# Kernel tuning notes

Hardware: AMD Instinct MI355X
Metric: run time of the kernel (lower is better)

The kernel has to match this reference:

```python
import jax, jax.numpy as jnp
import numpy as np

# dims: B=1 graph, N nodes, H heads, D head dim, M random features, K gumbel samples
N, E, H, D, M, K, IN = 50000, 800000, 4, 64, 30, 10, 128
TAU = 0.25
EPS = 1e-6


def _kernel_feat(data, proj, is_query):
    # FAVOR+ positive softmax kernel features. data [B,N,H,D], proj [M,D] -> [B,N,H,M]
    d = data.shape[-1]
    data = data * (float(d) ** -0.25)
    ratio = float(proj.shape[0]) ** -0.5
    dash = jnp.einsum('bnhd,md->bnhm', data, proj)
    diag = jnp.sum(data * data, axis=-1, keepdims=True) * 0.5
    if is_query:
        stab = jnp.max(dash, axis=-1, keepdims=True)
    else:
        stab = jnp.max(jnp.max(dash, axis=-1, keepdims=True), axis=-3, keepdims=True)
    return ratio * (jnp.exp(dash - diag - stab) + EPS)


def setup_inputs():
    key = jax.random.key(0)
    ks = jax.random.split(key, 10)
    def lin(k, o, i):
        return jax.random.normal(k, (o, i), jnp.float32) / np.sqrt(i)
    return {
        'z': jax.random.normal(ks[0], (1, N, IN), jnp.float32),
        'edge_index': jax.random.randint(ks[1], (2, E), 0, N),
        'Wq_w': lin(ks[2], H * D, IN), 'Wq_b': jnp.zeros((H * D,), jnp.float32),
        'Wk_w': lin(ks[3], H * D, IN), 'Wk_b': jnp.zeros((H * D,), jnp.float32),
        'Wv_w': lin(ks[4], H * D, IN), 'Wv_b': jnp.zeros((H * D,), jnp.float32),
        'Wo_w': lin(ks[5], D, H * D), 'Wo_b': jnp.zeros((D,), jnp.float32),
        'b_rb': jnp.full((1, H), 0.1, jnp.float32),  # rb_order=1 relational-bias scalars
        'proj': jax.random.normal(ks[6], (M, D), jnp.float32),  # random-feature projection
        # pre-sampled Gumbel noise, already divided by tau and clamped at 20 as in torch
        'gumbels': jnp.minimum(jax.random.gumbel(ks[7], (N, 1, H, K), jnp.float32) / TAU, 20.0),
    }


def reference(z, edge_index, Wq_w, Wq_b, Wk_w, Wk_b, Wv_w, Wv_b, Wo_w, Wo_b, b_rb, proj, gumbels):
    B, Nn = z.shape[0], z.shape[1]
    inv_sqrt_tau = 1.0 / np.sqrt(TAU)
    q = (jnp.einsum('bni,oi->bno', z, Wq_w) + Wq_b).reshape(B, Nn, H, D)
    k = (jnp.einsum('bni,oi->bno', z, Wk_w) + Wk_b).reshape(B, Nn, H, D)
    v = (jnp.einsum('bni,oi->bno', z, Wv_w) + Wv_b).reshape(B, Nn, H, D)
    qp = jnp.transpose(_kernel_feat(q * inv_sqrt_tau, proj, True), (1, 0, 2, 3))   # [N,B,H,M]
    kp = jnp.transpose(_kernel_feat(k * inv_sqrt_tau, proj, False), (1, 0, 2, 3))  # [N,B,H,M]
    vp = jnp.transpose(v, (1, 0, 2, 3))                                             # [N,B,H,D]
    # Gumbel-perturbed keys: [N,B,H,K,M]
    ktg = kp[:, :, :, None, :] * jnp.exp(gumbels)[..., None]
    kvs = jnp.einsum('nbhkm,nbhd->bhkmd', ktg, vp)
    z_num = jnp.einsum('nbhm,bhkmd->nbhkd', qp, kvs)        # [N,B,H,K,D]
    z_den = jnp.einsum('nbhm,bhkm->nbhk', qp, jnp.sum(ktg, axis=0))
    z_next = jnp.transpose(jnp.mean(z_num / z_den[..., None], axis=3), (1, 0, 2, 3))  # [B,N,H,D]
    # edge attention weights A_weight [B,E,H]
    start, end = edge_index[0], edge_index[1]
    e_num = jnp.einsum('ebhm,ebhm->ebh', qp[end], kp[start])
    norm = jnp.einsum('nbhm,bhm->nbh', qp, jnp.sum(kp, axis=0))
    A_weight = jnp.transpose(e_num, (1, 0, 2)) / jnp.transpose(norm[end], (1, 0, 2))
    # relational bias (rb_order=1): sym-normalized sparse conv with per-head sigmoid scalar
    row, col = start, end
    d_in = jnp.zeros((Nn,), jnp.float32).at[col].add(1.0)
    d_out = jnp.zeros((Nn,), jnp.float32).at[row].add(1.0)
    coeff = jax.nn.sigmoid(b_rb[0])[None, :] * (jax.lax.rsqrt(d_in[col]) * jax.lax.rsqrt(d_out[row]))[:, None]  # [E,H]
    msg = v[0, row] * coeff[:, :, None]                      # [E,H,D]
    conv = jax.ops.segment_sum(msg, col, num_segments=Nn)[None]  # [1,N,H,D]
    z_next = z_next + conv
    out = jnp.einsum('bnf,of->bno', z_next.reshape(B, Nn, H * D), Wo_w) + Wo_b  # [B,N,D]
    return out, A_weight
```

## Files before the change

kernel.cpp:

```cpp
#include <hip/hip_runtime.h>

#define NN 50000
#define EE 800000
#define IND 128
#define NCOL 1024
#define KM 320
#define M30 30
#define RATIO 0.1825741858f
#define EPSF 1e-6f
#define QKSCALE 0.7071067812f
#define VTS 50176
#define KVSNB 196
#define AST 136

typedef __attribute__((ext_vector_type(8))) short bf16x8;
typedef __attribute__((ext_vector_type(4))) float f32x4;

__device__ __forceinline__ unsigned f2s(float f) {
    unsigned u = __float_as_uint(f);
    return (u & 0x80000000u) ? ~u : (u | 0x80000000u);
}
__device__ __forceinline__ float s2f(unsigned s) {
    return __uint_as_float((s & 0x80000000u) ? (s & 0x7fffffffu) : ~s);
}
__device__ __forceinline__ unsigned short f2bf(float f) {
    unsigned u = __float_as_uint(f);
    unsigned r = u + 0x7fffu + ((u >> 16) & 1u);
    return (unsigned short)(r >> 16);
}
__device__ __forceinline__ float bf2f(unsigned short h) {
    return __uint_as_float(((unsigned)h) << 16);
}

__global__ void k_prep(const float* __restrict__ Wq, const float* __restrict__ Wqb,
                       const float* __restrict__ Wk, const float* __restrict__ Wkb,
                       const float* __restrict__ Wv, const float* __restrict__ Wvb,
                       const float* __restrict__ Wo, const float* __restrict__ proj,
                       float* __restrict__ Wt, float* __restrict__ bext, float* __restrict__ WoT) {
    int i = blockIdx.x;
    int t = threadIdx.x;
    Wt[i*NCOL + t]       = QKSCALE * Wq[t*IND + i];
    Wt[i*NCOL + 256 + t] = QKSCALE * Wk[t*IND + i];
    Wt[i*NCOL + 512 + t] = Wv[t*IND + i];
    {
        const float* W = (t < 128) ? Wq : Wk;
        int c = (t < 128) ? t : (t - 128);
        int h = c >> 5, m = c & 31;
        float val = 0.f;
        if (m < M30) {
            for (int d = 0; d < 64; ++d)
                val += QKSCALE * W[(h*64+d)*IND + i] * proj[m*64 + d];
        }
        Wt[i*NCOL + 768 + t] = val;
    }
    if (t < 128) {
        int f = i*2 + (t >> 6);
        int o = t & 63;
        WoT[f*64 + o] = Wo[o*256 + f];
    }
    if (i == 0) {
        bext[t]       = QKSCALE * Wqb[t];
        bext[256 + t] = QKSCALE * Wkb[t];
        bext[512 + t] = Wvb[t];
        const float* Bb = (t < 128) ? Wqb : Wkb;
        int c = (t < 128) ? t : (t - 128);
        int h = c >> 5, m = c & 31;
        float val = 0.f;
        if (m < M30) {
            for (int d = 0; d < 64; ++d)
                val += QKSCALE * Bb[h*64+d] * proj[m*64 + d];
        }
        bext[768 + t] = val;
    }
}

__global__ void k_prep2(const float* __restrict__ Wt, unsigned short* __restrict__ Wcb) {
    int idx = blockIdx.x*256 + threadIdx.x;
    int col = idx >> 7, k = idx & 127;
    float f = Wt[k*NCOL + col];
    unsigned short hi = f2bf(f);
    unsigned short lo = f2bf(f - bf2f(hi));
    Wcb[col*128 + k] = hi;
    Wcb[131072 + col*128 + k] = lo;
}

__global__ void k_ztail(unsigned* __restrict__ vT32) {
    int idx = blockIdx.x*256 + threadIdx.x;
    int row = idx / 88, c = idx - row*88;
    vT32[(size_t)row * (VTS/2) + (50000/2) + c] = 0u;
}

__global__ __launch_bounds__(256) void k_qkv_mfma(const float* __restrict__ z,
                      const unsigned short* __restrict__ Wcb, const float* __restrict__ bext,
                      float* __restrict__ vbuf, float* __restrict__ qp, float* __restrict__ kpb,
                      unsigned* __restrict__ stab) {
    __shared__ __align__(16) unsigned short a_hi[128*AST];
    __shared__ float diag_l[2][4][128];
    int t = threadIdx.x;
    int n0 = blockIdx.x * 128;
    int w = t >> 6, lane = t & 63;
    #pragma unroll
    for (int half = 0; half < 2; ++half) {
        int node = (t >> 2) + half*64;
        int ks = (t & 3) * 32;
        bool ok = (n0 + node) < NN;
        const float* zr = z + (size_t)(n0 + node)*IND + ks;
        unsigned hbuf[16];
        #pragma unroll
        for (int c = 0; c < 8; ++c) {
            float4 v = ok ? *(const float4*)(zr + c*4) : make_float4(0.f,0.f,0.f,0.f);
            hbuf[c*2]   = (unsigned)f2bf(v.x) | ((unsigned)f2bf(v.y) << 16);
            hbuf[c*2+1] = (unsigned)f2bf(v.z) | ((unsigned)f2bf(v.w) << 16);
        }
        uint4* hp = (uint4*)(&a_hi[node*AST + ks]);
        #pragma unroll
        for (int c = 0; c < 4; ++c)
            hp[c] = make_uint4(hbuf[c*4], hbuf[c*4+1], hbuf[c*4+2], hbuf[c*4+3]);
    }
    __syncthreads();
    int arow = lane & 15;
    int ao = (lane >> 4) * 8;
    for (int c = 0; c < 4; ++c) {
        int colbase = c*256 + w*64;
        f32x4 acc[8][4];
        #pragma unroll
        for (int mt = 0; mt < 8; ++mt)
            #pragma unroll
            for (int nt = 0; nt < 4; ++nt)
                acc[mt][nt] = (f32x4){0.f,0.f,0.f,0.f};
        #pragma unroll
        for (int ks = 0; ks < 4; ++ks) {
            int ko = ks*32 + ao;
            bf16x8 Ah[8];
            #pragma unroll
            for (int mt = 0; mt < 8; ++mt)
                Ah[mt] = *(const bf16x8*)(&a_hi[(mt*16 + arow)*AST + ko]);
            #pragma unroll
            for (int nt = 0; nt < 4; ++nt) {
                const unsigned short* bp = Wcb + (size_t)(colbase + nt*16 + arow)*128 + ko;
                bf16x8 Bh = *(const bf16x8*)bp;
                bf16x8 Bl = *(const bf16x8*)(bp + 131072);
                #pragma unroll
                for (int mt = 0; mt < 8; ++mt) {
                    acc[mt][nt] = __builtin_amdgcn_mfma_f32_16x16x32_bf16(Ah[mt], Bh, acc[mt][nt], 0, 0, 0);
                    acc[mt][nt] = __builtin_amdgcn_mfma_f32_16x16x32_bf16(Ah[mt], Bl, acc[mt][nt], 0, 0, 0);
                }
            }
        }
        float bv[4];
        #pragma unroll
        for (int nt = 0; nt < 4; ++nt) bv[nt] = bext[colbase + nt*16 + arow];
        #pragma unroll
        for (int mt = 0; mt < 8; ++mt)
            #pragma unroll
            for (int nt = 0; nt < 4; ++nt)
                #pragma unroll
                for (int r = 0; r < 4; ++r)
                    acc[mt][nt][r] += bv[nt];
        if (c < 2) {
            #pragma unroll
            for (int mt = 0; mt < 8; ++mt) {
                #pragma unroll
                for (int r = 0; r < 4; ++r) {
                    float s = 0.f;
                    #pragma unroll
                    for (int nt = 0; nt < 4; ++nt) s += acc[mt][nt][r]*acc[mt][nt][r];
                    s += __shfl_xor(s, 1); s += __shfl_xor(s, 2);
                    s += __shfl_xor(s, 4); s += __shfl_xor(s, 8);
                    if (arow == 0) diag_l[c][w][mt*16 + (lane>>4)*4 + r] = 0.5f*s;
                }
            }
        } else if (c == 2) {
            #pragma unroll
            for (int mt = 0; mt < 8; ++mt)
                #pragma unroll
                for (int r = 0; r < 4; ++r) {
                    int node = n0 + mt*16 + (lane>>4)*4 + r;
                    if (node < NN) {
                        #pragma unroll
                        for (int nt = 0; nt < 4; ++nt)
                            vbuf[(size_t)node*256 + w*64 + nt*16 + arow] = acc[mt][nt][r];
                    }
                }
        } else {
            int hh = (w & 1) * 2;
            if (w < 2) {
                #pragma unroll
                for (int p = 0; p < 2; ++p) {
                    int h = hh + p;
                    #pragma unroll
                    for (int mt = 0; mt < 8; ++mt) {
                        #pragma unroll
                        for (int r = 0; r < 4; ++r) {
                            int row = mt*16 + (lane>>4)*4 + r;
                            float dg = diag_l[0][h][row];
                            float mx = fmaxf(acc[mt][2*p][r],
                                             (arow < 14) ? acc[mt][2*p+1][r] : -3.0e38f);
                            mx = fmaxf(mx, __shfl_xor(mx, 1)); mx = fmaxf(mx, __shfl_xor(mx, 2));
                            mx = fmaxf(mx, __shfl_xor(mx, 4)); mx = fmaxf(mx, __shfl_xor(mx, 8));
                            int node = n0 + row;
                            if (node < NN) {
                                #pragma unroll
                                for (int q2 = 0; q2 < 2; ++q2) {
                                    int m = q2*16 + arow;
                                    float val = 0.f;
                                    if (m < M30)
                                        val = RATIO * (__expf(acc[mt][2*p+q2][r] - dg - mx) + EPSF);
                                    qp[(size_t)node*128 + h*32 + m] = val;
                                }
                            }
                        }
                    }
                }
            } else {
                #pragma unroll
                for (int p = 0; p < 2; ++p) {
                    int h = hh + p;
                    float smax = -3.0e38f;
                    #pragma unroll
                    for (int mt = 0; mt < 8; ++mt) {
                        #pragma unroll
                        for (int r = 0; r < 4; ++r) {
                            int row = mt*16 + (lane>>4)*4 + r;
                            float dg = diag_l[1][h][row];
                            int node = n0 + row;
                            if (node < NN) {
                                #pragma unroll
                                for (int q2 = 0; q2 < 2; ++q2) {
                                    int m = q2*16 + arow;
                                    float d = acc[mt][2*p+q2][r];
                                    bool valid = (m < M30);
                                    kpb[(size_t)node*128 + h*32 + m] = valid ? (d - dg) : 0.f;
                                    if (valid) smax = fmaxf(smax, d);
                                }
                            }
                        }
                    }
                    smax = fmaxf(smax, __shfl_xor(smax, 1));  smax = fmaxf(smax, __shfl_xor(smax, 2));
                    smax = fmaxf(smax, __shfl_xor(smax, 4));  smax = fmaxf(smax, __shfl_xor(smax, 8));
                    smax = fmaxf(smax, __shfl_xor(smax, 16)); smax = fmaxf(smax, __shfl_xor(smax, 32));
                    if (lane == 0) atomicMax(&stab[h], f2s(smax));
                }
            }
        }
        __syncthreads();
    }
}

__global__ __launch_bounds__(256) void k_vt(const float* __restrict__ vbuf,
                      unsigned short* __restrict__ vT) {
    __shared__ unsigned short tile[64][72];
    int t = threadIdx.x;
    int n0 = blockIdx.x * 64;
    int c0 = blockIdx.y * 64;
    {
        int node = t >> 2, cs = (t & 3) * 16;
        bool ok = (n0 + node) < NN;
        const float* vr = vbuf + (size_t)(n0 + node)*256 + c0 + cs;
        #pragma unroll
        for (int cc = 0; cc < 4; ++cc) {
            float4 v = ok ? *(const float4*)(vr + cc*4) : make_float4(0.f,0.f,0.f,0.f);
            unsigned u0 = (unsigned)f2bf(v.x) | ((unsigned)f2bf(v.y) << 16);
            unsigned u1 = (unsigned)f2bf(v.z) | ((unsigned)f2bf(v.w) << 16);
            *(unsigned*)(&tile[node][cs + cc*4])     = u0;
            *(unsigned*)(&tile[node][cs + cc*4 + 2]) = u1;
        }
    }
    __syncthreads();
    {
        int d = t >> 2, ns = (t & 3) * 16;
        unsigned ob[8];
        #pragma unroll
        for (int i = 0; i < 8; ++i) {
            unsigned short a = tile[ns + i*2][d];
            unsigned short b = tile[ns + i*2 + 1][d];
            ob[i] = (unsigned)a | ((unsigned)b << 16);
        }
        unsigned short* op = vT + (size_t)(c0 + d)*VTS + n0 + ns;
        *(uint4*)(op)     = make_uint4(ob[0], ob[1], ob[2], ob[3]);
        *(uint4*)(op + 8) = make_uint4(ob[4], ob[5], ob[6], ob[7]);
    }
}

__global__ void k_deg(const int* __restrict__ ei, int* __restrict__ din, int* __restrict__ dout) {
    int e = blockIdx.x*256 + threadIdx.x;
    if (e < EE) {
        atomicAdd(&dout[ei[e]], 1);
        atomicAdd(&din[ei[EE + e]], 1);
    }
}

__global__ void k_scan_part(const int* __restrict__ din, int* __restrict__ bsum) {
    __shared__ int red[256];
    int t = threadIdx.x;
    int i = blockIdx.x*256 + t;
    red[t] = (i < NN) ? din[i] : 0;
    __syncthreads();
    for (int off = 128; off >= 1; off >>= 1) {
        if (t < off) red[t] += red[t+off];
        __syncthreads();
    }
    if (t == 0) bsum[blockIdx.x] = red[0];
}
__global__ void k_scan_top(const int* __restrict__ bsum, int* __restrict__ boff) {
    if (threadIdx.x == 0) {
        int acc = 0;
        for (int b = 0; b < 196; ++b) { boff[b] = acc; acc += bsum[b]; }
    }
}
__global__ void k_scan_fin(const int* __restrict__ din, const int* __restrict__ boff,
                           int* __restrict__ offsets, int* __restrict__ cursor,
                           const int* __restrict__ dout_, float* __restrict__ rsd) {
    __shared__ int s[256];
    int t = threadIdx.x;
    int i = blockIdx.x*256 + t;
    if (i < NN) {
        int d = dout_[i];
        rsd[i] = d > 0 ? rsqrtf((float)d) : 0.f;
    }
    int v = (i < NN) ? din[i] : 0;
    s[t] = v;
    __syncthreads();
    for (int off = 1; off < 256; off <<= 1) {
        int add = (t >= off) ? s[t-off] : 0;
        __syncthreads();
        s[t] += add;
        __syncthreads();
    }
    int excl = s[t] - v + boff[blockIdx.x];
    if (i < NN) { offsets[i] = excl; cursor[i] = excl; }
    if (i == NN-1) offsets[NN] = excl + v;
}

__global__ void k_scatter(const int* __restrict__ ei, int* __restrict__ cursor,
                          int2* __restrict__ csr_pack) {
    int e = blockIdx.x*256 + threadIdx.x;
    if (e < EE) {
        int col = ei[EE + e];
        int pos = atomicAdd(&cursor[col], 1);
        csr_pack[pos] = make_int2(ei[e], e);
    }
}

__global__ void k_kp(const float* __restrict__ kpb, const unsigned* __restrict__ stab,
                     float* __restrict__ kp_sum, unsigned short* __restrict__ kp_bf) {
    __shared__ float red[256];
    int t = threadIdx.x;
    int hm = t & 127;
    int h = hm >> 5, m = hm & 31;
    float st = s2f(stab[h]);
    float ksum = 0.f;
    const int total = NN*128;
    for (int idx = blockIdx.x*256 + t; idx < total; idx += gridDim.x*256) {
        float val = kpb[idx];
        float kpv = 0.f;
        if (m < M30) kpv = RATIO * (__expf(val - st) + EPSF);
        kp_bf[idx] = f2bf(kpv);
        ksum += kpv;
    }
    red[t] = ksum;
    __syncthreads();
    if (t < 128) atomicAdd(&kp_sum[hm], red[t] + red[t+128]);
}

__global__ __launch_bounds__(256) void k_kvs(const unsigned short* __restrict__ kp_bf,
                      const float* __restrict__ g, const unsigned short* __restrict__ vT,
                      float* __restrict__ kvs, float* __restrict__ ktg) {
    __shared__ __align__(16) unsigned short w_l[320*40];
    __shared__ __align__(16) unsigned short v_l[64*40];
    __shared__ __align__(16) float eg_l[10][36];
    __shared__ float kp_lf[32][33];
    int t = threadIdx.x;
    int h = blockIdx.y;
    int n0b = blockIdx.x * 256;
    int lane = t & 63;
    int wb = (t >> 6) * 80;
    int arow = lane & 15;
    int acol = (lane >> 4) * 8;
    f32x4 acc[5][4];
    #pragma unroll
    for (int kt = 0; kt < 5; ++kt)
        #pragma unroll
        for (int dt = 0; dt < 4; ++dt)
            acc[kt][dt] = (f32x4){0.f, 0.f, 0.f, 0.f};
    float wsum0 = 0.f, wsum1 = 0.f;
    int k0 = t >> 5, m0 = t & 31;
    int k1 = 8 + (t >> 5), m1 = t & 31;

    for (int st = 0; st < 8; ++st) {
        int n0 = n0b + st * 32;
        __syncthreads();
        #pragma unroll
        for (int i = 0; i < 2; ++i) {
            int flat = t + i*256;
            if (flat < 320) {
                int kk = flat % 10, n = flat / 10;
                float e = 0.f;
                if (n0 + n < NN) e = __expf(g[(size_t)(n0+n)*40 + h*10 + kk]);
                eg_l[kk][n] = e;
            }
        }
        {
            int d = t >> 2, seg = t & 3;
            uint4 vv = *(const uint4*)(vT + (size_t)(h*64 + d)*VTS + n0 + seg*8);
            *(uint4*)(&v_l[d*40 + seg*8]) = vv;
        }
        if (t < 128) {
            int n = t >> 2, seg = t & 3;
            int gn = n0 + n;
            if (gn < NN) {
                uint4 kv = *(const uint4*)(kp_bf + (size_t)gn*128 + h*32 + seg*8);
                unsigned uu[4] = {kv.x, kv.y, kv.z, kv.w};
                #pragma unroll
                for (int j = 0; j < 4; ++j) {
                    kp_lf[n][seg*8 + j*2]     = __uint_as_float(uu[j] << 16);
                    kp_lf[n][seg*8 + j*2 + 1] = __uint_as_float(uu[j] & 0xFFFF0000u);
                }
            } else {
                #pragma unroll
                for (int j = 0; j < 8; ++j) kp_lf[n][seg*8 + j] = 0.f;
            }
        }
        __syncthreads();
        {
            {
                unsigned dw[16];
                float s = 0.f;
                #pragma unroll
                for (int c = 0; c < 16; ++c) {
                    float kpa = kp_lf[c*2][m0];
                    float kpc = kp_lf[c*2+1][m0];
                    unsigned ua = __float_as_uint(kpa * eg_l[k0][c*2]);
                    unsigned ub = __float_as_uint(kpc * eg_l[k0][c*2+1]);
                    s += __uint_as_float(ua & 0xFFFF0000u) + __uint_as_float(ub & 0xFFFF0000u);
                    dw[c] = (ua >> 16) | (ub & 0xFFFF0000u);
                }
                wsum0 += s;
                uint4* wp = (uint4*)(&w_l[t*40]);
                wp[0] = make_uint4(dw[0], dw[1], dw[2],  dw[3]);
                wp[1] = make_uint4(dw[4], dw[5], dw[6],  dw[7]);
                wp[2] = make_uint4(dw[8], dw[9], dw[10], dw[11]);
                wp[3] = make_uint4(dw[12],dw[13],dw[14], dw[15]);
            }
            if (t < 64) {
                unsigned dw[16];
                float s = 0.f;
                #pragma unroll
                for (int c = 0; c < 16; ++c) {
                    float kpa = kp_lf[c*2][m1];
                    float kpc = kp_lf[c*2+1][m1];
                    unsigned ua = __float_as_uint(kpa * eg_l[k1][c*2]);
                    unsigned ub = __float_as_uint(kpc * eg_l[k1][c*2+1]);
                    s += __uint_as_float(ua & 0xFFFF0000u) + __uint_as_float(ub & 0xFFFF0000u);
                    dw[c] = (ua >> 16) | (ub & 0xFFFF0000u);
                }
                wsum1 += s;
                uint4* wp = (uint4*)(&w_l[(t + 256)*40]);
                wp[0] = make_uint4(dw[0], dw[1], dw[2],  dw[3]);
                wp[1] = make_uint4(dw[4], dw[5], dw[6],  dw[7]);
                wp[2] = make_uint4(dw[8], dw[9], dw[10], dw[11]);
                wp[3] = make_uint4(dw[12],dw[13],dw[14], dw[15]);
            }
        }
        __syncthreads();
        bf16x8 Bf[4];
        #pragma unroll
        for (int dt = 0; dt < 4; ++dt)
            Bf[dt] = *(const bf16x8*)(&v_l[(dt*16 + arow)*40 + acol]);
        #pragma unroll
        for (int kt = 0; kt < 5; ++kt) {
            bf16x8 Af = *(const bf16x8*)(&w_l[(wb + kt*16 + arow)*40 + acol]);
            #pragma unroll
            for (int dt = 0; dt < 4; ++dt)
                acc[kt][dt] = __builtin_amdgcn_mfma_f32_16x16x32_bf16(Af, Bf[dt], acc[kt][dt], 0, 0, 0);
        }
    }
    {
        int orow = (lane >> 4) * 4;
        int ocol = lane & 15;
        float* kb = kvs + h*KM*64;
        #pragma unroll
        for (int kt = 0; kt < 5; ++kt)
            #pragma unroll
            for (int dt = 0; dt < 4; ++dt)
                #pragma unroll
                for (int r = 0; r < 4; ++r)
                    atomicAdd(&kb[(wb + kt*16 + orow + r)*64 + dt*16 + ocol], acc[kt][dt][r]);
        atomicAdd(&ktg[h*KM + t], wsum0);
        if (t < 64) atomicAdd(&ktg[h*KM + 256 + t], wsum1);
    }
}

__global__ __launch_bounds__(256) void k_znext(const float* __restrict__ qp, const float* __restrict__ kvs,
                        const float* __restrict__ ktg, const float* __restrict__ kp_sum,
                        float* __restrict__ znext, unsigned short* __restrict__ qpn_bf) {
    int t = threadIdx.x;
    int n = blockIdx.x*256 + t;
    int h = blockIdx.y;
    if (n >= NN) return;
    float q[32];
    const float* qb = qp + (size_t)n*128 + h*32;
    #pragma unroll
    for (int c = 0; c < 8; ++c) {
        float4 v4 = *(const float4*)(qb + c*4);
        q[c*4+0]=v4.x; q[c*4+1]=v4.y; q[c*4+2]=v4.z; q[c*4+3]=v4.w;
    }
    const float* ks = kp_sum + h*32;
    float norm = 0.f;
    #pragma unroll
    for (int m = 0; m < 32; ++m) norm = fmaf(q[m], ks[m], norm);
    float rn = 1.f / norm;
    #pragma unroll
    for (int m = 0; m < 32; ++m) q[m] *= rn;
    {
        unsigned ob[16];
        #pragma unroll
        for (int c = 0; c < 16; ++c)
            ob[c] = (unsigned)f2bf(q[c*2]) | ((unsigned)f2bf(q[c*2+1]) << 16);
        unsigned short* qo = qpn_bf + (size_t)n*128 + h*32;
        *(uint4*)(qo)      = make_uint4(ob[0],  ob[1],  ob[2],  ob[3]);
        *(uint4*)(qo + 8)  = make_uint4(ob[4],  ob[5],  ob[6],  ob[7]);
        *(uint4*)(qo + 16) = make_uint4(ob[8],  ob[9],  ob[10], ob[11]);
        *(uint4*)(qo + 24) = make_uint4(ob[12], ob[13], ob[14], ob[15]);
    }
    const float* kvh = kvs + h*KM*64;
    const float* kth = ktg + h*KM;
    float* zo = znext + (size_t)n*256 + h*64;
    for (int dc = 0; dc < 4; ++dc) {
        float ms[16];
        #pragma unroll
        for (int d = 0; d < 16; ++d) ms[d] = 0.f;
        for (int k = 0; k < 10; ++k) {
            float den = 0.f;
            #pragma unroll
            for (int m = 0; m < 32; ++m) den = fmaf(q[m], kth[k*32+m], den);
            float rd = 1.f / (den * 10.f);
            const float* base = kvh + k*2048 + dc*16;
            #pragma unroll
            for (int m = 0; m < 32; ++m) {
                float qm = q[m] * rd;
                #pragma unroll
                for (int d = 0; d < 16; ++d)
                    ms[d] = fmaf(qm, base[m*64 + d], ms[d]);
            }
        }
        #pragma unroll
        for (int d = 0; d < 16; ++d) zo[dc*16 + d] = ms[d];
    }
}

__global__ __launch_bounds__(256) void k_convedge(const int* __restrict__ offsets,
                        const int2* __restrict__ csr_pack,
                        const int* __restrict__ din, const unsigned short* __restrict__ vr,
                        const unsigned short* __restrict__ kp_bf,
                        const unsigned short* __restrict__ qpn_bf,
                        const float* __restrict__ brb, float* __restrict__ znext,
                        float* __restrict__ A) {
    __shared__ unsigned short qpn_l[4][128];
    int t = threadIdx.x;
    int w = t >> 6, lane = t & 63;
    int col = blockIdx.x*4 + w;
    if (lane < 8) {
        uint4 q4 = *(const uint4*)(qpn_bf + (size_t)col*128 + lane*8);
        *(uint4*)(&qpn_l[w][lane*8]) = q4;
    }
    __syncthreads();
    int s0 = offsets[col], s1 = offsets[col+1];
    int hq = (lane & 31) >> 3;
    float qv0, qv1, qv2, qv3;
    {
        ushort4 qq = *(const ushort4*)(&qpn_l[w][hq*32 + (lane & 7)*4]);
        qv0 = bf2f(qq.x); qv1 = bf2f(qq.y); qv2 = bf2f(qq.z); qv3 = bf2f(qq.w);
    }
    bool dowrite = (lane < 32) && ((lane & 7) == 0);
    float a0 = 0.f, a1 = 0.f, a2 = 0.f, a3 = 0.f;
    int j = s0;
    for (; j + 2 <= s1; j += 2) {
        int2 p0 = csr_pack[j];
        int2 p1 = csr_pack[j+1];
        ushort4 u0 = *(const ushort4*)(vr + (size_t)p0.x*256 + lane*4);
        ushort4 u1 = *(const ushort4*)(vr + (size_t)p1.x*256 + lane*4);
        ushort4 k0 = *(const ushort4*)(kp_bf + (size_t)p0.x*128 + (lane & 31)*4);
        ushort4 k1 = *(const ushort4*)(kp_bf + (size_t)p1.x*128 + (lane & 31)*4);
        a0 += bf2f(u0.x) + bf2f(u1.x);
        a1 += bf2f(u0.y) + bf2f(u1.y);
        a2 += bf2f(u0.z) + bf2f(u1.z);
        a3 += bf2f(u0.w) + bf2f(u1.w);
        float d0 = qv0*bf2f(k0.x) + qv1*bf2f(k0.y) + qv2*bf2f(k0.z) + qv3*bf2f(k0.w);
        float d1 = qv0*bf2f(k1.x) + qv1*bf2f(k1.y) + qv2*bf2f(k1.z) + qv3*bf2f(k1.w);
        d0 += __shfl_xor(d0, 1); d1 += __shfl_xor(d1, 1);
        d0 += __shfl_xor(d0, 2); d1 += __shfl_xor(d1, 2);
        d0 += __shfl_xor(d0, 4); d1 += __shfl_xor(d1, 4);
        if (dowrite) {
            A[(size_t)p0.y*4 + hq] = d0;
            A[(size_t)p1.y*4 + hq] = d1;
        }
    }
    if (j < s1) {
        int2 p0 = csr_pack[j];
        ushort4 u0 = *(const ushort4*)(vr + (size_t)p0.x*256 + lane*4);
        ushort4 k0 = *(const ushort4*)(kp_bf + (size_t)p0.x*128 + (lane & 31)*4);
        a0 += bf2f(u0.x); a1 += bf2f(u0.y); a2 += bf2f(u0.z); a3 += bf2f(u0.w);
        float d0 = qv0*bf2f(k0.x) + qv1*bf2f(k0.y) + qv2*bf2f(k0.z) + qv3*bf2f(k0.w);
        d0 += __shfl_xor(d0, 1); d0 += __shfl_xor(d0, 2); d0 += __shfl_xor(d0, 4);
        if (dowrite) A[(size_t)p0.y*4 + hq] = d0;
    }
    if (s0 == s1) return;
    int h = lane >> 4;
    float sig = 1.f / (1.f + __expf(-brb[h]));
    float sc = sig * rsqrtf((float)din[col]);
    float* zp = znext + (size_t)col*256 + lane*4;
    float4 zv = *(float4*)zp;
    zv.x += sc*a0; zv.y += sc*a1; zv.z += sc*a2; zv.w += sc*a3;
    *(float4*)zp = zv;
}

__global__ __launch_bounds__(256) void k_vr(const float* __restrict__ vbuf,
                      const float* __restrict__ rsd, unsigned short* __restrict__ vr) {
    int t = threadIdx.x;
    int row = blockIdx.x*4 + (t >> 6);
    int lane = t & 63;
    float rs = rsd[row];
    float4 v4 = *(const float4*)(vbuf + (size_t)row*256 + lane*4);
    ushort4 o;
    o.x = f2bf(rs * v4.x);
    o.y = f2bf(rs * v4.y);
    o.z = f2bf(rs * v4.z);
    o.w = f2bf(rs * v4.w);
    *(ushort4*)(vr + (size_t)row*256 + lane*4) = o;
}

__global__ __launch_bounds__(256) void k_out(const float* __restrict__ znext, const float* __restrict__ WoT,
                      const float* __restrict__ Wob, float* __restrict__ out) {
    int n = blockIdx.x*256 + threadIdx.x;
    if (n >= NN) return;
    float acc[64];
    #pragma unroll
    for (int o = 0; o < 64; ++o) acc[o] = Wob[o];
    const float* zr = znext + (size_t)n*256;
    for (int fc = 0; fc < 64; ++fc) {
        float4 z4 = *(const float4*)(zr + fc*4);
        float zz[4] = {z4.x, z4.y, z4.z, z4.w};
        #pragma unroll
        for (int j = 0; j < 4; ++j) {
            const float* wr = WoT + (fc*4+j)*64;
            #pragma unroll
            for (int o = 0; o < 64; ++o)
                acc[o] = fmaf(zz[j], wr[o], acc[o]);
        }
    }
    float* ob = out + (size_t)n*64;
    #pragma unroll
    for (int o = 0; o < 64; ++o) ob[o] = acc[o];
}

extern "C" void kernel_launch(void* const* d_in, const int* in_sizes, int n_in,
                              void* d_out, int out_size, void* d_ws, size_t ws_size,
                              hipStream_t stream) {
    const float* z    = (const float*)d_in[0];
    const int*   ei   = (const int*)d_in[1];
    const float* Wq   = (const float*)d_in[2];
    const float* Wqb  = (const float*)d_in[3];
    const float* Wk   = (const float*)d_in[4];
    const float* Wkb  = (const float*)d_in[5];
    const float* Wv   = (const float*)d_in[6];
    const float* Wvb  = (const float*)d_in[7];
    const float* Wo   = (const float*)d_in[8];
    const float* Wob  = (const float*)d_in[9];
    const float* brb  = (const float*)d_in[10];
    const float* proj = (const float*)d_in[11];
    const float* g    = (const float*)d_in[12];
    float* out = (float*)d_out;
    float* A   = out + (size_t)NN*64;
    float* ws  = (float*)d_ws;

    float* Wt      = ws;
    float* bext    = ws + 131072;
    float* WoT     = ws + 132096;
    float* kvs     = ws + 148480;
    float* ktg     = ws + 230400;
    float* kp_sum  = ws + 231680;
    unsigned* stab = (unsigned*)(ws + 231808);
    int* din       = (int*)(ws + 231812);
    int* dout_     = (int*)(ws + 281812);
    float* vbuf    = ws + 331840;
    float* qp      = ws + 13131840;
    float* kpb     = ws + 19531840;
    float* znext   = ws + 25931840;
    int* offsets   = (int*)(ws + 38731840);
    int* cursor    = (int*)(ws + 38781844);
    int* bsum      = (int*)(ws + 38831844);
    int* boff      = (int*)(ws + 38832040);
    float* rsd     = ws + 38832236;
    unsigned short* Wcb = (unsigned short*)(ws + 38882240);
    unsigned short* vT     = (unsigned short*)znext;
    int2* csr_pack         = (int2*)kpb;
    float* A_scratch       = kpb + 1600000;
    unsigned short* vr     = (unsigned short*)qp;
    unsigned short* kp_bf  = (unsigned short*)A;
    unsigned short* qpn_bf = (unsigned short*)out;

    hipMemsetAsync(ws + 148480, 0, (size_t)(331840 - 148480)*sizeof(float), stream);
    k_prep<<<128, 256, 0, stream>>>(Wq, Wqb, Wk, Wkb, Wv, Wvb, Wo, proj, Wt, bext, WoT);
    k_prep2<<<512, 256, 0, stream>>>(Wt, Wcb);
    k_ztail<<<88, 256, 0, stream>>>((unsigned*)vT);
    k_qkv_mfma<<<391, 256, 0, stream>>>(z, Wcb, bext, vbuf, qp, kpb, stab);
    k_deg<<<3125, 256, 0, stream>>>(ei, din, dout_);
    k_scan_part<<<196, 256, 0, stream>>>(din, bsum);
    k_scan_top<<<1, 64, 0, stream>>>(bsum, boff);
    k_scan_fin<<<196, 256, 0, stream>>>(din, boff, offsets, cursor, dout_, rsd);
    k_kp<<<512, 256, 0, stream>>>(kpb, stab, kp_sum, kp_bf);
    k_scatter<<<3125, 256, 0, stream>>>(ei, cursor, csr_pack);
    k_vt<<<dim3(782, 4), 256, 0, stream>>>(vbuf, vT);
    k_kvs<<<dim3(KVSNB, 4), 256, 0, stream>>>(kp_bf, g, vT, kvs, ktg);
    k_znext<<<dim3(196,4), 256, 0, stream>>>(qp, kvs, ktg, kp_sum, znext, qpn_bf);
    k_vr<<<12500, 256, 0, stream>>>(vbuf, rsd, vr);
    k_convedge<<<12500, 256, 0, stream>>>(offsets, csr_pack, din, vr, kp_bf,
                                          qpn_bf, brb, znext, A_scratch);
    k_out<<<196, 256, 0, stream>>>(znext, WoT, Wob, out);
    hipMemcpyAsync(A, A_scratch, (size_t)EE*4*sizeof(float), hipMemcpyDeviceToDevice, stream);
}
```

Measured before the change: 756.2 us.

## Compute z_next numerator with bf16 MFMA over scaled query features

Replaces the scalar per-node k_znext loop with an MFMA kernel. Each block builds a 64-node tile of per-sample scaled query features (q/den) in bf16 shared memory and multiplies it against a transposed bf16 copy of kvs produced by a new small conversion kernel. The mean over the K samples folds into the 320-long reduction. This targets a large FMA-bound loop with heavy redundant loads of kvs, at the cost of bf16 rounding of kvs and of the scaled queries, plus one extra launch.

```diff
diff --git a/kernel.cpp b/kernel.cpp
--- a/kernel.cpp
+++ b/kernel.cpp
@@ -491,61 +491,98 @@
     }
 }
 
-__global__ __launch_bounds__(256) void k_znext(const float* __restrict__ qp, const float* __restrict__ kvs,
+__global__ void k_kvsbf(const float* __restrict__ kvs, unsigned short* __restrict__ kvs_bfT) {
+    int idx = blockIdx.x*256 + threadIdx.x;
+    int h = idx / 20480;
+    int rem = idx - h*20480;
+    int d = rem / 320;
+    int km = rem - d*320;
+    kvs_bfT[idx] = f2bf(kvs[(size_t)h*20480 + km*64 + d]);
+}
+
+__global__ __launch_bounds__(256) void k_znext_mfma(const float* __restrict__ qp,
+                        const unsigned short* __restrict__ kvs_bfT,
                         const float* __restrict__ ktg, const float* __restrict__ kp_sum,
                         float* __restrict__ znext, unsigned short* __restrict__ qpn_bf) {
-    int t = threadIdx.x;
-    int n = blockIdx.x*256 + t;
+    __shared__ __align__(16) unsigned short A_l[64*328];
+    __shared__ float ktg_l[320];
+    __shared__ float ksum_l[32];
+    int t = threadIdx.x;
     int h = blockIdx.y;
-    if (n >= NN) return;
-    float q[32];
-    const float* qb = qp + (size_t)n*128 + h*32;
-    #pragma unroll
-    for (int c = 0; c < 8; ++c) {
-        float4 v4 = *(const float4*)(qb + c*4);
-        q[c*4+0]=v4.x; q[c*4+1]=v4.y; q[c*4+2]=v4.z; q[c*4+3]=v4.w;
-    }
-    const float* ks = kp_sum + h*32;
-    float norm = 0.f;
-    #pragma unroll
-    for (int m = 0; m < 32; ++m) norm = fmaf(q[m], ks[m], norm);
-    float rn = 1.f / norm;
-    #pragma unroll
-    for (int m = 0; m < 32; ++m) q[m] *= rn;
+    int n0 = blockIdx.x * 64;
+    ktg_l[t] = ktg[h*KM + t];
+    if (t < 64) ktg_l[256 + t] = ktg[h*KM + 256 + t];
+    if (t < 32) ksum_l[t] = kp_sum[h*32 + t];
+    __syncthreads();
     {
-        unsigned ob[16];
-        #pragma unroll
-        for (int c = 0; c < 16; ++c)
-            ob[c] = (unsigned)f2bf(q[c*2]) | ((unsigned)f2bf(q[c*2+1]) << 16);
-        unsigned short* qo = qpn_bf + (size_t)n*128 + h*32;
-        *(uint4*)(qo)      = make_uint4(ob[0],  ob[1],  ob[2],  ob[3]);
-        *(uint4*)(qo + 8)  = make_uint4(ob[4],  ob[5],  ob[6],  ob[7]);
-        *(uint4*)(qo + 16) = make_uint4(ob[8],  ob[9],  ob[10], ob[11]);
-        *(uint4*)(qo + 24) = make_uint4(ob[12], ob[13], ob[14], ob[15]);
-    }
-    const float* kvh = kvs + h*KM*64;
-    const float* kth = ktg + h*KM;
-    float* zo = znext + (size_t)n*256 + h*64;
-    for (int dc = 0; dc < 4; ++dc) {
-        float ms[16];
-        #pragma unroll
-        for (int d = 0; d < 16; ++d) ms[d] = 0.f;
+        int node = t >> 2, p = t & 3;
+        int n = n0 + node;
+        bool ok = (n < NN);
+        float q8[8];
+        if (ok) {
+            const float* qb = qp + (size_t)n*128 + h*32 + p*8;
+            float4 a = *(const float4*)(qb);
+            float4 b = *(const float4*)(qb + 4);
+            q8[0]=a.x; q8[1]=a.y; q8[2]=a.z; q8[3]=a.w;
+            q8[4]=b.x; q8[5]=b.y; q8[6]=b.z; q8[7]=b.w;
+        } else {
+            #pragma unroll
+            for (int j = 0; j < 8; ++j) q8[j] = 0.f;
+        }
+        float part = 0.f;
+        #pragma unroll
+        for (int j = 0; j < 8; ++j) part = fmaf(q8[j], ksum_l[p*8 + j], part);
+        part += __shfl_xor(part, 1); part += __shfl_xor(part, 2);
+        float rn = ok ? (1.f / part) : 0.f;
+        #pragma unroll
+        for (int j = 0; j < 8; ++j) q8[j] *= rn;
+        if (ok) {
+            unsigned ob[4];
+            #pragma unroll
+            for (int c = 0; c < 4; ++c)
+                ob[c] = (unsigned)f2bf(q8[c*2]) | ((unsigned)f2bf(q8[c*2+1]) << 16);
+            *(uint4*)(qpn_bf + (size_t)n*128 + h*32 + p*8) = make_uint4(ob[0], ob[1], ob[2], ob[3]);
+        }
+        #pragma unroll
         for (int k = 0; k < 10; ++k) {
-            float den = 0.f;
-            #pragma unroll
-            for (int m = 0; m < 32; ++m) den = fmaf(q[m], kth[k*32+m], den);
-            float rd = 1.f / (den * 10.f);
-            const float* base = kvh + k*2048 + dc*16;
-            #pragma unroll
-            for (int m = 0; m < 32; ++m) {
-                float qm = q[m] * rd;
-                #pragma unroll
-                for (int d = 0; d < 16; ++d)
-                    ms[d] = fmaf(qm, base[m*64 + d], ms[d]);
-            }
-        }
-        #pragma unroll
-        for (int d = 0; d < 16; ++d) zo[dc*16 + d] = ms[d];
+            float dp = 0.f;
+            #pragma unroll
+            for (int j = 0; j < 8; ++j) dp = fmaf(q8[j], ktg_l[k*32 + p*8 + j], dp);
+            dp += __shfl_xor(dp, 1); dp += __shfl_xor(dp, 2);
+            float rd = ok ? (1.f / (dp * 10.f)) : 0.f;
+            unsigned ob[4];
+            #pragma unroll
+            for (int c = 0; c < 4; ++c)
+                ob[c] = (unsigned)f2bf(q8[c*2]*rd) | ((unsigned)f2bf(q8[c*2+1]*rd) << 16);
+            *(uint4*)(&A_l[node*328 + k*32 + p*8]) = make_uint4(ob[0], ob[1], ob[2], ob[3]);
+        }
+    }
+    __syncthreads();
+    {
+        int lane = t & 63, w = t >> 6;
+        int arow = lane & 15;
+        int ao = (lane >> 4) * 8;
+        f32x4 acc[4];
+        #pragma unroll
+        for (int mt = 0; mt < 4; ++mt) acc[mt] = (f32x4){0.f,0.f,0.f,0.f};
+        const unsigned short* Bb = kvs_bfT + (size_t)h*20480 + (w*16 + arow)*320;
+        #pragma unroll
+        for (int ks = 0; ks < 10; ++ks) {
+            bf16x8 Bf = *(const bf16x8*)(Bb + ks*32 + ao);
+            #pragma unroll
+            for (int mt = 0; mt < 4; ++mt) {
+                bf16x8 Af = *(const bf16x8*)(&A_l[(mt*16 + arow)*328 + ks*32 + ao]);
+                acc[mt] = __builtin_amdgcn_mfma_f32_16x16x32_bf16(Af, Bf, acc[mt], 0, 0, 0);
+            }
+        }
+        #pragma unroll
+        for (int mt = 0; mt < 4; ++mt)
+            #pragma unroll
+            for (int r = 0; r < 4; ++r) {
+                int n = n0 + mt*16 + (lane>>4)*4 + r;
+                if (n < NN)
+                    znext[(size_t)n*256 + h*64 + w*16 + arow] = acc[mt][r];
+            }
     }
 }
 
@@ -693,6 +730,7 @@
     int* boff      = (int*)(ws + 38832040);
     float* rsd     = ws + 38832236;
     unsigned short* Wcb = (unsigned short*)(ws + 38882240);
+    unsigned short* kvs_bfT = (unsigned short*)(ws + 39013312);
     unsigned short* vT     = (unsigned short*)znext;
     int2* csr_pack         = (int2*)kpb;
     float* A_scratch       = kpb + 1600000;
@@ -713,7 +751,8 @@
     k_scatter<<<3125, 256, 0, stream>>>(ei, cursor, csr_pack);
     k_vt<<<dim3(782, 4), 256, 0, stream>>>(vbuf, vT);
     k_kvs<<<dim3(KVSNB, 4), 256, 0, stream>>>(kp_bf, g, vT, kvs, ktg);
-    k_znext<<<dim3(196,4), 256, 0, stream>>>(qp, kvs, ktg, kp_sum, znext, qpn_bf);
+    k_kvsbf<<<320, 256, 0, stream>>>(kvs, kvs_bfT);
+    k_znext_mfma<<<dim3(782, 4), 256, 0, stream>>>(qp, kvs_bfT, ktg, kp_sum, znext, qpn_bf);
     k_vr<<<12500, 256, 0, stream>>>(vbuf, rsd, vr);
     k_convedge<<<12500, 256, 0, stream>>>(offsets, csr_pack, din, vr, kp_bf,
                                           qpn_bf, brb, znext, A_scratch);
```

Measured after the change: 657.3 us, median of 2. -13.1%, faster.
